# Performance work log

Hardware: AMD Instinct MI355X
Metric: run time of the kernel (lower is better)

Reference implementation:

```python
import jax, jax.numpy as jnp
import numpy as np

N_NODES = 100000
N_EDGES = 1600000
D_IN, D_HID, D_OUT = 256, 512, 48
K_STEPS = 10
ALPHA = 0.1


def setup_inputs() -> dict:
    key = jax.random.key(0)
    k_x, k_e, k_w1, k_w2 = jax.random.split(key, 4)
    x = jax.random.normal(k_x, (N_NODES, D_IN), dtype=jnp.float32)
    edge_index = jax.random.randint(k_e, (2, N_EDGES), 0, N_NODES, dtype=jnp.int64)
    # MLP params (Kaiming-ish scaling)
    W1 = jax.random.normal(k_w1, (D_IN, D_HID), dtype=jnp.float32) * (1.0 / np.sqrt(D_IN))
    b1 = jnp.zeros((D_HID,), dtype=jnp.float32)
    W2 = jax.random.normal(k_w2, (D_HID, D_OUT), dtype=jnp.float32) * (1.0 / np.sqrt(D_HID))
    b2 = jnp.zeros((D_OUT,), dtype=jnp.float32)
    return {"x": x, "edge_index": edge_index, "W1": W1, "b1": b1, "W2": W2, "b2": b2}


def reference(x, edge_index, W1, b1, W2, b2):
    N = x.shape[0]
    # --- MLP encoder ---
    h = jax.nn.relu(x @ W1 + b1) @ W2 + b2  # [N, D_OUT]

    # --- APPNP propagation (PyG defaults: add self-loops, symmetric gcn_norm) ---
    loop = jnp.arange(N, dtype=edge_index.dtype)
    src = jnp.concatenate([edge_index[0], loop])  # [E+N]
    dst = jnp.concatenate([edge_index[1], loop])
    ones = jnp.ones(src.shape[0], dtype=h.dtype)
    deg = jax.ops.segment_sum(ones, dst, num_segments=N)  # in-degree incl. self-loop
    dinv = jnp.where(deg > 0, jax.lax.rsqrt(deg), 0.0)
    norm = dinv[src] * dinv[dst]  # [E+N]

    out = h
    for _ in range(K_STEPS):
        msg = out[src] * norm[:, None]                      # gather + scale
        agg = jax.ops.segment_sum(msg, dst, num_segments=N)  # scatter-add
        out = (1.0 - ALPHA) * agg + ALPHA * h                # teleport mix
    return out
```

## Files before the change

### kernel.cpp

```cpp
#include <hip/hip_runtime.h>
#include <hip/hip_fp16.h>

constexpr int D_IN = 256, D_HID = 512, D_OUT = 48;
constexpr int HPAD = 64;
constexpr int K_STEPS = 10;

typedef __attribute__((ext_vector_type(8))) __bf16 bf16x8;
typedef __attribute__((ext_vector_type(4))) float f32x4;

__device__ __forceinline__ unsigned short f2bf(float f) {
  unsigned u = __builtin_bit_cast(unsigned, f);
  u += 0x7fffu + ((u >> 16) & 1u);
  return (unsigned short)(u >> 16);
}


__global__ void zero2_kernel(int* __restrict__ a, int* __restrict__ b, int N) {
  int i = blockIdx.x * 256 + threadIdx.x;
  if (i < N) { a[i] = 0; b[i] = 0; }
}

__global__ void count_kernel(const int* __restrict__ dst, int* __restrict__ cnt, int E) {
  int e = blockIdx.x * 256 + threadIdx.x;
  if (e < E) atomicAdd(&cnt[dst[e]], 1);
}

__global__ void dinv_kernel(const int* __restrict__ cnt, float* __restrict__ dinv, int N) {
  int n = blockIdx.x * 256 + threadIdx.x;
  if (n < N) dinv[n] = rsqrtf((float)(cnt[n] + 1));
}

__global__ void scan1_kernel(const int* __restrict__ cnt, int* __restrict__ row_ptr,
                             int* __restrict__ bsum, int N) {
  __shared__ int sd[256];
  int tid = threadIdx.x, b = blockIdx.x;
  int i0 = b * 1024 + tid * 4;
  int v[4];
#pragma unroll
  for (int m = 0; m < 4; ++m) v[m] = (i0 + m < N) ? ((cnt[i0 + m] + 3) & ~3) : 0;
  int s = v[0] + v[1] + v[2] + v[3];
  sd[tid] = s;
  __syncthreads();
  for (int off = 1; off < 256; off <<= 1) {
    int t = (tid >= off) ? sd[tid - off] : 0;
    __syncthreads();
    sd[tid] += t;
    __syncthreads();
  }
  int run = sd[tid] - s;
#pragma unroll
  for (int m = 0; m < 4; ++m) {
    if (i0 + m < N) row_ptr[i0 + m] = run;
    run += v[m];
  }
  if (tid == 255) bsum[b] = sd[255];
}

__global__ void scan2_kernel(const int* __restrict__ bsum, int* __restrict__ bofs,
                             int* __restrict__ row_ptr, int NB, int N) {
  __shared__ int sd[128];
  int tid = threadIdx.x;
  int v = (tid < NB) ? bsum[tid] : 0;
  sd[tid] = v;
  __syncthreads();
  for (int off = 1; off < 128; off <<= 1) {
    int t = (tid >= off) ? sd[tid - off] : 0;
    __syncthreads();
    sd[tid] += t;
    __syncthreads();
  }
  if (tid < NB) bofs[tid] = sd[tid] - v;
  if (tid == 127) row_ptr[N] = sd[127];
}

__global__ void scan3_kernel(int* __restrict__ row_ptr, const int* __restrict__ bofs, int N) {
  int b = blockIdx.x;
  if (b == 0) return;
  int add = bofs[b];
  int i0 = b * 1024 + threadIdx.x * 4;
#pragma unroll
  for (int m = 0; m < 4; ++m)
    if (i0 + m < N) row_ptr[i0 + m] += add;
}

__global__ void fill_kernel(const int* __restrict__ src, const int* __restrict__ dst,
                            const int* __restrict__ row_ptr, int* __restrict__ cnt2,
                            const float* __restrict__ dinv,
                            int2* __restrict__ edges, int E) {
  int e = blockIdx.x * 256 + threadIdx.x;
  if (e >= E) return;
  int s = src[e], d = dst[e];
  int p = row_ptr[d] + atomicAdd(&cnt2[d], 1);
  edges[p] = make_int2(s, __float_as_int(dinv[s]));
}

__global__ void pad_kernel(const int* __restrict__ cnt, const int* __restrict__ row_ptr,
                           int2* __restrict__ edges, int N) {
  int n = blockIdx.x * 256 + threadIdx.x;
  if (n >= N) return;
  int a = row_ptr[n] + cnt[n];
  int b = row_ptr[n + 1];
  for (int p = a; p < b; ++p) edges[p] = make_int2(n, 0);
}


__global__ void convert_w1(const float* __restrict__ W1, unsigned short* __restrict__ W1T) {
  int i = blockIdx.x * 256 + threadIdx.x;
  if (i >= D_HID * D_IN) return;
  int c = i >> 8, k = i & 255;
  W1T[i] = f2bf(W1[k * D_HID + c]);
}

__global__ void convert_w2(const float* __restrict__ W2, unsigned short* __restrict__ W2T) {
  int i = blockIdx.x * 256 + threadIdx.x;
  if (i >= D_OUT * D_HID) return;
  int n = i >> 9, k = i & 511;
  W2T[i] = f2bf(W2[k * D_OUT + n]);
}


__global__ __launch_bounds__(256, 3) void encoder_kernel(
    const float* __restrict__ x, const float* __restrict__ b1,
    const float* __restrict__ b2,
    const unsigned short* __restrict__ W1T,
    const unsigned short* __restrict__ W2T,
    __half* __restrict__ h2, int N) {
  __shared__ unsigned short sB[64][136];
  __shared__ unsigned short sHid[128][72];
  __shared__ unsigned short sW2[48][72];

  int tid = threadIdx.x;
  int w = tid >> 6, lane = tid & 63;
  int q = lane >> 4, l15 = lane & 15;
  int row0 = blockIdx.x * 128;
  int m0 = w * 16;

  bf16x8 axf[2][8];
#pragma unroll
  for (int mt = 0; mt < 2; ++mt) {
    int grow = row0 + mt * 64 + m0 + l15;
    bool rok = grow < N;
    const float* xr = x + (size_t)grow * D_IN;
#pragma unroll
    for (int jb = 0; jb < 8; ++jb) {
      float4 v0 = make_float4(0.f, 0.f, 0.f, 0.f), v1 = v0;
      if (rok) {
        v0 = *(const float4*)(xr + jb * 32 + q * 8);
        v1 = *(const float4*)(xr + jb * 32 + q * 8 + 4);
      }
      union { bf16x8 v; unsigned short s[8]; } u;
      u.s[0] = f2bf(v0.x); u.s[1] = f2bf(v0.y); u.s[2] = f2bf(v0.z); u.s[3] = f2bf(v0.w);
      u.s[4] = f2bf(v1.x); u.s[5] = f2bf(v1.y); u.s[6] = f2bf(v1.z); u.s[7] = f2bf(v1.w);
      axf[mt][jb] = u.v;
    }
  }

  f32x4 hacc[2][3];
#pragma unroll
  for (int mt = 0; mt < 2; ++mt)
#pragma unroll
    for (int t = 0; t < 3; ++t)
#pragma unroll
      for (int r = 0; r < 4; ++r) hacc[mt][t][r] = 0.f;

  for (int ct = 0; ct < 8; ++ct) {
    int c0 = ct * 64;
    f32x4 acc[2][4];
#pragma unroll
    for (int mt = 0; mt < 2; ++mt)
#pragma unroll
      for (int t = 0; t < 4; ++t)
#pragma unroll
        for (int r = 0; r < 4; ++r) acc[mt][t][r] = 0.f;

#pragma unroll
    for (int kh = 0; kh < 2; ++kh) {
      __syncthreads();
#pragma unroll
      for (int i = 0; i < 4; ++i) {
        int id = i * 256 + tid;
        int r = id >> 4, c = id & 15;
        *(uint4*)&sB[r][c * 8] =
            *(const uint4*)(W1T + (size_t)(c0 + r) * D_IN + kh * 128 + c * 8);
      }
      if (kh == 0) {
        int r = tid >> 3, c8 = tid & 7;
        *(uint4*)&sW2[r][c8 * 8] = *(const uint4*)(W2T + (size_t)r * D_HID + c0 + c8 * 8);
        int id = 256 + tid;
        if (id < 384) {
          int r2 = id >> 3, c2 = id & 7;
          *(uint4*)&sW2[r2][c2 * 8] = *(const uint4*)(W2T + (size_t)r2 * D_HID + c0 + c2 * 8);
        }
      }
      __syncthreads();
#pragma unroll
      for (int kb = 0; kb < 4; ++kb) {
#pragma unroll
        for (int tn = 0; tn < 4; ++tn) {
          bf16x8 b = *(const bf16x8*)&sB[tn * 16 + l15][kb * 32 + q * 8];
          acc[0][tn] = __builtin_amdgcn_mfma_f32_16x16x32_bf16(axf[0][kh * 4 + kb], b, acc[0][tn], 0, 0, 0);
          acc[1][tn] = __builtin_amdgcn_mfma_f32_16x16x32_bf16(axf[1][kh * 4 + kb], b, acc[1][tn], 0, 0, 0);
        }
      }
    }
#pragma unroll
    for (int mt = 0; mt < 2; ++mt)
#pragma unroll
      for (int tn = 0; tn < 4; ++tn) {
        int c = tn * 16 + l15;
        float bias = b1[c0 + c];
#pragma unroll
        for (int rg = 0; rg < 4; ++rg) {
          float v = acc[mt][tn][rg] + bias;
          v = v > 0.f ? v : 0.f;
          sHid[mt * 64 + m0 + q * 4 + rg][c] = f2bf(v);
        }
      }
#pragma unroll
    for (int kk = 0; kk < 2; ++kk) {
      bf16x8 a0 = *(const bf16x8*)&sHid[m0 + l15][kk * 32 + q * 8];
      bf16x8 a1 = *(const bf16x8*)&sHid[64 + m0 + l15][kk * 32 + q * 8];
#pragma unroll
      for (int tn = 0; tn < 3; ++tn) {
        bf16x8 b = *(const bf16x8*)&sW2[tn * 16 + l15][kk * 32 + q * 8];
        hacc[0][tn] = __builtin_amdgcn_mfma_f32_16x16x32_bf16(a0, b, hacc[0][tn], 0, 0, 0);
        hacc[1][tn] = __builtin_amdgcn_mfma_f32_16x16x32_bf16(a1, b, hacc[1][tn], 0, 0, 0);
      }
    }
  }
#pragma unroll
  for (int mt = 0; mt < 2; ++mt) {
#pragma unroll
    for (int tn = 0; tn < 3; ++tn) {
      int c = tn * 16 + l15;
      float bias = b2[c];
#pragma unroll
      for (int rg = 0; rg < 4; ++rg) {
        int gr = row0 + mt * 64 + m0 + q * 4 + rg;
        if (gr < N) h2[(size_t)gr * HPAD + c] = __float2half(hacc[mt][tn][rg] + bias);
      }
    }
#pragma unroll
    for (int rg = 0; rg < 4; ++rg) {
      int gr = row0 + mt * 64 + m0 + q * 4 + rg;
      if (gr < N) h2[(size_t)gr * HPAD + 48 + l15] = __float2half(0.f);
    }
  }
}


__global__ __launch_bounds__(256) void prop_kernel(
    const __half* __restrict__ cur, const __half* __restrict__ h2,
    const float* __restrict__ dinv, const int* __restrict__ row_ptr,
    const int2* __restrict__ edges, __half* __restrict__ nxt,
    float* __restrict__ outf, int N, int last) {
  int wid = (blockIdx.x * 256 + threadIdx.x) >> 6;
  int lane = threadIdx.x & 63;
  int half = lane >> 5;
  int slot = (lane >> 3) & 3;
  int s = lane & 7;
  int node = wid * 2 + half;
  bool nok = node < N;
  int p0 = 0, p1 = 0;
  if (nok) { int2 pp = *(const int2*)(row_ptr + node); p0 = pp.x; p1 = pp.y; }
  int d = p1 - p0;
  int dmax = max(d, __shfl_xor(d, 32));
  int nb = dmax >> 2;

  float acc[8];
#pragma unroll
  for (int i = 0; i < 8; ++i) acc[i] = 0.f;

  int p = p0 + slot;
  int2 er = make_int2(0, 0);
  if (nb > 0) er = edges[p];
  for (int b = 0; b < nb; ++b) {
    float wgt = (p < p1) ? __int_as_float(er.y) : 0.f;
    int sn = er.x;
    int2 ern = er;
    if (b + 1 < nb) ern = edges[p + 4];
    union { float4 f; __half2 h[4]; } u;
    u.f = *(const float4*)(cur + ((size_t)sn << 6) + s * 8);
#pragma unroll
    for (int i = 0; i < 4; ++i) {
      float2 f = __half22float2(u.h[i]);
      acc[2 * i]     += wgt * f.x;
      acc[2 * i + 1] += wgt * f.y;
    }
    er = ern; p += 4;
  }
#pragma unroll
  for (int i = 0; i < 8; ++i) {
    acc[i] += __int_as_float(__builtin_amdgcn_ds_swizzle(__float_as_int(acc[i]), 0x201F));
    acc[i] += __int_as_float(__builtin_amdgcn_ds_swizzle(__float_as_int(acc[i]), 0x401F));
  }
  if ((lane & 24) != 0 || !nok) return;
  float di = dinv[node];
  size_t base = ((size_t)node << 6) + s * 8;
  union { float4 f; __half2 h[4]; } us, uh;
  us.f = *(const float4*)(cur + base);
  uh.f = *(const float4*)(h2 + base);
  float dii = di * di;
  float outv[8];
#pragma unroll
  for (int i = 0; i < 4; ++i) {
    float2 sf = __half22float2(us.h[i]);
    float2 hf = __half22float2(uh.h[i]);
    outv[2 * i]     = 0.9f * (di * acc[2 * i]     + dii * sf.x) + 0.1f * hf.x;
    outv[2 * i + 1] = 0.9f * (di * acc[2 * i + 1] + dii * sf.y) + 0.1f * hf.y;
  }
  if (last) {
    if (s < 6) {
      float* op = outf + (size_t)node * D_OUT + s * 8;
      *(float4*)op       = make_float4(outv[0], outv[1], outv[2], outv[3]);
      *(float4*)(op + 4) = make_float4(outv[4], outv[5], outv[6], outv[7]);
    }
  } else {
    union { uint4 u4; __half2 h[4]; } o;
#pragma unroll
    for (int i = 0; i < 4; ++i) o.h[i] = __floats2half2_rn(outv[2 * i], outv[2 * i + 1]);
    *(uint4*)(nxt + base) = o.u4;
  }
}


extern "C" void kernel_launch(void* const* d_in, const int* in_sizes, int n_in,
                              void* d_out, int out_size, void* d_ws, size_t ws_size,
                              hipStream_t stream) {
  (void)n_in; (void)out_size; (void)ws_size;
  const float* x  = (const float*)d_in[0];
  const int*   ei = (const int*)d_in[1];
  const float* W1 = (const float*)d_in[2];
  const float* b1 = (const float*)d_in[3];
  const float* W2 = (const float*)d_in[4];
  const float* b2 = (const float*)d_in[5];
  const int N = in_sizes[0] / D_IN;
  const int E = in_sizes[1] / 2;
  const int* e_src = ei;
  const int* e_dst = ei + E;

  char* ws = (char*)d_ws;
  size_t off = 0;
  auto take = [&](size_t bytes) -> char* {
    char* p = ws + off;
    off += (bytes + 511) & ~(size_t)511;
    return p;
  };
  int* cnt      = (int*)take((size_t)N * 4);
  int* cnt2     = (int*)take((size_t)N * 4);
  float* dinv   = (float*)take((size_t)N * 4);
  int* row_ptr  = (int*)take((size_t)(N + 1) * 4);
  int* bsum     = (int*)take(1024);
  int* bofs     = (int*)take(1024);
  int2* edges   = (int2*)take(((size_t)E + 4 * (size_t)N) * 8);
  unsigned short* W1T = (unsigned short*)take((size_t)D_IN * D_HID * 2);
  unsigned short* W2T = (unsigned short*)take((size_t)D_HID * D_OUT * 2);
  __half* h2    = (__half*)take((size_t)N * HPAD * 2);
  __half* bufA  = (__half*)take((size_t)N * HPAD * 2);
  __half* bufB  = (__half*)d_out;
  float* outp   = (float*)d_out;

  int nb256 = (N + 255) / 256;
  int eb256 = (E + 255) / 256;
  int NB    = (N + 1023) / 1024;

  zero2_kernel<<<nb256, 256, 0, stream>>>(cnt, cnt2, N);
  count_kernel<<<eb256, 256, 0, stream>>>(e_dst, cnt, E);
  dinv_kernel<<<nb256, 256, 0, stream>>>(cnt, dinv, N);
  scan1_kernel<<<NB, 256, 0, stream>>>(cnt, row_ptr, bsum, N);
  scan2_kernel<<<1, 128, 0, stream>>>(bsum, bofs, row_ptr, NB, N);
  scan3_kernel<<<NB, 256, 0, stream>>>(row_ptr, bofs, N);
  fill_kernel<<<eb256, 256, 0, stream>>>(e_src, e_dst, row_ptr, cnt2, dinv, edges, E);
  pad_kernel<<<nb256, 256, 0, stream>>>(cnt, row_ptr, edges, N);

  convert_w1<<<(D_IN * D_HID + 255) / 256, 256, 0, stream>>>(W1, W1T);
  convert_w2<<<(D_HID * D_OUT + 255) / 256, 256, 0, stream>>>(W2, W2T);
  encoder_kernel<<<(N + 127) / 128, 256, 0, stream>>>(x, b1, b2, W1T, W2T, h2, N);

  int waves = (N + 1) / 2;
  int pblocks = (waves + 3) / 4;
  const __half* src = h2;
  __half* dst = bufA;
  for (int it = 1; it <= K_STEPS; ++it) {
    int last = (it == K_STEPS);
    prop_kernel<<<pblocks, 256, 0, stream>>>(src, h2, dinv, row_ptr, edges,
                                             dst, outp, N, last);
    src = dst;
    dst = (dst == bufA) ? bufB : bufA;
  }
}
```

Before: 749.0 us.

## Drop feature padding to 48 halves, pre-cast x to bf16, prefetch encoder weights

Node feature buffers shrink from a 64-half padded stride to a dense 48-half stride. Each propagation gather now reads 12 bytes per lane instead of 16, and the gather loop is unrolled by two edges to keep more loads in flight. The input x is converted to bf16 in a separate kernel before the encoder, and the encoder's W1/W2 tile loads are software-prefetched into registers one stage ahead. The pre-cast adds an extra full pass over x (read fp32, write bf16). The uint3 loads are narrower and not 16-byte aligned, which may lower gather efficiency.

```diff
diff --git a/kernel.cpp b/kernel.cpp
--- a/kernel.cpp
+++ b/kernel.cpp
@@ -2,7 +2,6 @@
 #include <hip/hip_fp16.h>
 
 constexpr int D_IN = 256, D_HID = 512, D_OUT = 48;
-constexpr int HPAD = 64;
 constexpr int K_STEPS = 10;
 
 typedef __attribute__((ext_vector_type(8))) __bf16 bf16x8;
@@ -104,6 +103,17 @@
 }
 
 
+__global__ void xcast_kernel(const float* __restrict__ x,
+                             unsigned short* __restrict__ xb, int total8) {
+  int i = blockIdx.x * 256 + threadIdx.x;
+  if (i >= total8) return;
+  const float4* p = (const float4*)(x + (size_t)i * 8);
+  float4 a = p[0], b = p[1];
+  unsigned short o[8] = {f2bf(a.x), f2bf(a.y), f2bf(a.z), f2bf(a.w),
+                         f2bf(b.x), f2bf(b.y), f2bf(b.z), f2bf(b.w)};
+  *(uint4*)(xb + (size_t)i * 8) = *(const uint4*)o;
+}
+
 __global__ void convert_w1(const float* __restrict__ W1, unsigned short* __restrict__ W1T) {
   int i = blockIdx.x * 256 + threadIdx.x;
   if (i >= D_HID * D_IN) return;
@@ -120,8 +130,8 @@
 
 
 __global__ __launch_bounds__(256, 3) void encoder_kernel(
-    const float* __restrict__ x, const float* __restrict__ b1,
-    const float* __restrict__ b2,
+    const unsigned short* __restrict__ xb,
+    const float* __restrict__ b1, const float* __restrict__ b2,
     const unsigned short* __restrict__ W1T,
     const unsigned short* __restrict__ W2T,
     __half* __restrict__ h2, int N) {
@@ -134,102 +144,112 @@
   int q = lane >> 4, l15 = lane & 15;
   int row0 = blockIdx.x * 128;
   int m0 = w * 16;
-
-  bf16x8 axf[2][8];
+  int sr = tid >> 4, sc = tid & 15;
+  int w2r0 = tid >> 3, w2c0 = tid & 7;
+  int w2id1 = 256 + tid;
+
+  uint4 axu[2][8];
 #pragma unroll
   for (int mt = 0; mt < 2; ++mt) {
     int grow = row0 + mt * 64 + m0 + l15;
     bool rok = grow < N;
-    const float* xr = x + (size_t)grow * D_IN;
-#pragma unroll
-    for (int jb = 0; jb < 8; ++jb) {
-      float4 v0 = make_float4(0.f, 0.f, 0.f, 0.f), v1 = v0;
-      if (rok) {
-        v0 = *(const float4*)(xr + jb * 32 + q * 8);
-        v1 = *(const float4*)(xr + jb * 32 + q * 8 + 4);
+    const unsigned short* xr = xb + (size_t)grow * D_IN;
+#pragma unroll
+    for (int jb = 0; jb < 8; ++jb)
+      axu[mt][jb] = rok ? *(const uint4*)(xr + jb * 32 + q * 8)
+                        : make_uint4(0, 0, 0, 0);
+  }
+
+  uint4 pre[4], w2p[2];
+#pragma unroll
+  for (int i = 0; i < 4; ++i)
+    pre[i] = *(const uint4*)(W1T + (size_t)(sr + i * 16) * D_IN + sc * 8);
+  w2p[0] = *(const uint4*)(W2T + (size_t)w2r0 * D_HID + w2c0 * 8);
+  if (w2id1 < 384)
+    w2p[1] = *(const uint4*)(W2T + (size_t)(w2id1 >> 3) * D_HID + (w2id1 & 7) * 8);
+
+  f32x4 hacc[2][3];
+#pragma unroll
+  for (int mt = 0; mt < 2; ++mt)
+#pragma unroll
+    for (int t = 0; t < 3; ++t)
+#pragma unroll
+      for (int r = 0; r < 4; ++r) hacc[mt][t][r] = 0.f;
+
+  f32x4 acc[2][4];
+  for (int st = 0; st < 16; ++st) {
+    int ct = st >> 1, kh = st & 1;
+    int c0 = ct * 64;
+    __syncthreads();
+#pragma unroll
+    for (int i = 0; i < 4; ++i)
+      *(uint4*)&sB[sr + i * 16][sc * 8] = pre[i];
+    if (kh == 0) {
+      *(uint4*)&sW2[w2r0][w2c0 * 8] = w2p[0];
+      if (w2id1 < 384) *(uint4*)&sW2[w2id1 >> 3][(w2id1 & 7) * 8] = w2p[1];
+    }
+    __syncthreads();
+    if (st < 15) {
+      int ct2 = (st + 1) >> 1, kh2 = (st + 1) & 1;
+      const unsigned short* wb = W1T + (size_t)(ct2 * 64) * D_IN + kh2 * 128;
+#pragma unroll
+      for (int i = 0; i < 4; ++i)
+        pre[i] = *(const uint4*)(wb + (size_t)(sr + i * 16) * D_IN + sc * 8);
+      if (kh2 == 0) {
+        int c02 = ct2 * 64;
+        w2p[0] = *(const uint4*)(W2T + (size_t)w2r0 * D_HID + c02 + w2c0 * 8);
+        if (w2id1 < 384)
+          w2p[1] = *(const uint4*)(W2T + (size_t)(w2id1 >> 3) * D_HID + c02 + (w2id1 & 7) * 8);
       }
-      union { bf16x8 v; unsigned short s[8]; } u;
-      u.s[0] = f2bf(v0.x); u.s[1] = f2bf(v0.y); u.s[2] = f2bf(v0.z); u.s[3] = f2bf(v0.w);
-      u.s[4] = f2bf(v1.x); u.s[5] = f2bf(v1.y); u.s[6] = f2bf(v1.z); u.s[7] = f2bf(v1.w);
-      axf[mt][jb] = u.v;
-    }
-  }
-
-  f32x4 hacc[2][3];
-#pragma unroll
-  for (int mt = 0; mt < 2; ++mt)
-#pragma unroll
-    for (int t = 0; t < 3; ++t)
-#pragma unroll
-      for (int r = 0; r < 4; ++r) hacc[mt][t][r] = 0.f;
-
-  for (int ct = 0; ct < 8; ++ct) {
-    int c0 = ct * 64;
-    f32x4 acc[2][4];
-#pragma unroll
-    for (int mt = 0; mt < 2; ++mt)
-#pragma unroll
-      for (int t = 0; t < 4; ++t)
-#pragma unroll
-        for (int r = 0; r < 4; ++r) acc[mt][t][r] = 0.f;
-
-#pragma unroll
-    for (int kh = 0; kh < 2; ++kh) {
-      __syncthreads();
-#pragma unroll
-      for (int i = 0; i < 4; ++i) {
-        int id = i * 256 + tid;
-        int r = id >> 4, c = id & 15;
-        *(uint4*)&sB[r][c * 8] =
-            *(const uint4*)(W1T + (size_t)(c0 + r) * D_IN + kh * 128 + c * 8);
+    }
+    if (kh == 0) {
+#pragma unroll
+      for (int mt = 0; mt < 2; ++mt)
+#pragma unroll
+        for (int t = 0; t < 4; ++t)
+#pragma unroll
+          for (int r = 0; r < 4; ++r) acc[mt][t][r] = 0.f;
+    }
+#pragma unroll
+    for (int kb = 0; kb < 4; ++kb) {
+      bf16x8 a0 = __builtin_bit_cast(bf16x8, axu[0][kh * 4 + kb]);
+      bf16x8 a1 = __builtin_bit_cast(bf16x8, axu[1][kh * 4 + kb]);
+#pragma unroll
+      for (int tn = 0; tn < 4; ++tn) {
+        bf16x8 b = *(const bf16x8*)&sB[tn * 16 + l15][kb * 32 + q * 8];
+        acc[0][tn] = __builtin_amdgcn_mfma_f32_16x16x32_bf16(a0, b, acc[0][tn], 0, 0, 0);
+        acc[1][tn] = __builtin_amdgcn_mfma_f32_16x16x32_bf16(a1, b, acc[1][tn], 0, 0, 0);
       }
-      if (kh == 0) {
-        int r = tid >> 3, c8 = tid & 7;
-        *(uint4*)&sW2[r][c8 * 8] = *(const uint4*)(W2T + (size_t)r * D_HID + c0 + c8 * 8);
-        int id = 256 + tid;
-        if (id < 384) {
-          int r2 = id >> 3, c2 = id & 7;
-          *(uint4*)&sW2[r2][c2 * 8] = *(const uint4*)(W2T + (size_t)r2 * D_HID + c0 + c2 * 8);
+    }
+    if (kh == 1) {
+#pragma unroll
+      for (int mt = 0; mt < 2; ++mt)
+#pragma unroll
+        for (int tn = 0; tn < 4; ++tn) {
+          int c = tn * 16 + l15;
+          float bias = b1[c0 + c];
+#pragma unroll
+          for (int rg = 0; rg < 4; ++rg) {
+            float v = acc[mt][tn][rg] + bias;
+            v = v > 0.f ? v : 0.f;
+            sHid[mt * 64 + m0 + q * 4 + rg][c] = f2bf(v);
+          }
+        }
+#pragma unroll
+      for (int kk = 0; kk < 2; ++kk) {
+        bf16x8 a0 = *(const bf16x8*)&sHid[m0 + l15][kk * 32 + q * 8];
+        bf16x8 a1 = *(const bf16x8*)&sHid[64 + m0 + l15][kk * 32 + q * 8];
+#pragma unroll
+        for (int tn = 0; tn < 3; ++tn) {
+          bf16x8 b = *(const bf16x8*)&sW2[tn * 16 + l15][kk * 32 + q * 8];
+          hacc[0][tn] = __builtin_amdgcn_mfma_f32_16x16x32_bf16(a0, b, hacc[0][tn], 0, 0, 0);
+          hacc[1][tn] = __builtin_amdgcn_mfma_f32_16x16x32_bf16(a1, b, hacc[1][tn], 0, 0, 0);
         }
       }
-      __syncthreads();
-#pragma unroll
-      for (int kb = 0; kb < 4; ++kb) {
-#pragma unroll
-        for (int tn = 0; tn < 4; ++tn) {
-          bf16x8 b = *(const bf16x8*)&sB[tn * 16 + l15][kb * 32 + q * 8];
-          acc[0][tn] = __builtin_amdgcn_mfma_f32_16x16x32_bf16(axf[0][kh * 4 + kb], b, acc[0][tn], 0, 0, 0);
-          acc[1][tn] = __builtin_amdgcn_mfma_f32_16x16x32_bf16(axf[1][kh * 4 + kb], b, acc[1][tn], 0, 0, 0);
-        }
-      }
-    }
-#pragma unroll
-    for (int mt = 0; mt < 2; ++mt)
-#pragma unroll
-      for (int tn = 0; tn < 4; ++tn) {
-        int c = tn * 16 + l15;
-        float bias = b1[c0 + c];
-#pragma unroll
-        for (int rg = 0; rg < 4; ++rg) {
-          float v = acc[mt][tn][rg] + bias;
-          v = v > 0.f ? v : 0.f;
-          sHid[mt * 64 + m0 + q * 4 + rg][c] = f2bf(v);
-        }
-      }
-#pragma unroll
-    for (int kk = 0; kk < 2; ++kk) {
-      bf16x8 a0 = *(const bf16x8*)&sHid[m0 + l15][kk * 32 + q * 8];
-      bf16x8 a1 = *(const bf16x8*)&sHid[64 + m0 + l15][kk * 32 + q * 8];
-#pragma unroll
-      for (int tn = 0; tn < 3; ++tn) {
-        bf16x8 b = *(const bf16x8*)&sW2[tn * 16 + l15][kk * 32 + q * 8];
-        hacc[0][tn] = __builtin_amdgcn_mfma_f32_16x16x32_bf16(a0, b, hacc[0][tn], 0, 0, 0);
-        hacc[1][tn] = __builtin_amdgcn_mfma_f32_16x16x32_bf16(a1, b, hacc[1][tn], 0, 0, 0);
-      }
-    }
-  }
-#pragma unroll
-  for (int mt = 0; mt < 2; ++mt) {
+    }
+  }
+#pragma unroll
+  for (int mt = 0; mt < 2; ++mt)
 #pragma unroll
     for (int tn = 0; tn < 3; ++tn) {
       int c = tn * 16 + l15;
@@ -237,17 +257,20 @@
 #pragma unroll
       for (int rg = 0; rg < 4; ++rg) {
         int gr = row0 + mt * 64 + m0 + q * 4 + rg;
-        if (gr < N) h2[(size_t)gr * HPAD + c] = __float2half(hacc[mt][tn][rg] + bias);
+        if (gr < N) h2[(size_t)gr * D_OUT + c] = __float2half(hacc[mt][tn][rg] + bias);
       }
     }
-#pragma unroll
-    for (int rg = 0; rg < 4; ++rg) {
-      int gr = row0 + mt * 64 + m0 + q * 4 + rg;
-      if (gr < N) h2[(size_t)gr * HPAD + 48 + l15] = __float2half(0.f);
-    }
-  }
-}
-
+}
+
+
+__device__ __forceinline__ void fma6(float* acc, float wgt, uint3 g) {
+  float2 f0 = __half22float2(__builtin_bit_cast(__half2, g.x));
+  float2 f1 = __half22float2(__builtin_bit_cast(__half2, g.y));
+  float2 f2 = __half22float2(__builtin_bit_cast(__half2, g.z));
+  acc[0] += wgt * f0.x; acc[1] += wgt * f0.y;
+  acc[2] += wgt * f1.x; acc[3] += wgt * f1.y;
+  acc[4] += wgt * f2.x; acc[5] += wgt * f2.y;
+}
 
 __global__ __launch_bounds__(256) void prop_kernel(
     const __half* __restrict__ cur, const __half* __restrict__ h2,
@@ -267,59 +290,68 @@
   int dmax = max(d, __shfl_xor(d, 32));
   int nb = dmax >> 2;
 
-  float acc[8];
-#pragma unroll
-  for (int i = 0; i < 8; ++i) acc[i] = 0.f;
+  float acc[6];
+#pragma unroll
+  for (int i = 0; i < 6; ++i) acc[i] = 0.f;
 
   int p = p0 + slot;
-  int2 er = make_int2(0, 0);
-  if (nb > 0) er = edges[p];
-  for (int b = 0; b < nb; ++b) {
-    float wgt = (p < p1) ? __int_as_float(er.y) : 0.f;
-    int sn = er.x;
-    int2 ern = er;
-    if (b + 1 < nb) ern = edges[p + 4];
-    union { float4 f; __half2 h[4]; } u;
-    u.f = *(const float4*)(cur + ((size_t)sn << 6) + s * 8);
-#pragma unroll
-    for (int i = 0; i < 4; ++i) {
-      float2 f = __half22float2(u.h[i]);
-      acc[2 * i]     += wgt * f.x;
-      acc[2 * i + 1] += wgt * f.y;
-    }
-    er = ern; p += 4;
-  }
-#pragma unroll
-  for (int i = 0; i < 8; ++i) {
+  int2 e0 = make_int2(0, 0), e1 = make_int2(0, 0);
+  if (nb > 0) e0 = edges[p];
+  if (nb > 1) e1 = edges[p + 4];
+  int b = 0;
+  for (; b + 2 <= nb; b += 2) {
+    int2 n0 = make_int2(0, 0), n1 = make_int2(0, 0);
+    if (b + 2 < nb) n0 = edges[p + 8];
+    if (b + 3 < nb) n1 = edges[p + 12];
+    float w0 = (p < p1) ? __int_as_float(e0.y) : 0.f;
+    float w1 = (p + 4 < p1) ? __int_as_float(e1.y) : 0.f;
+    uint3 g0 = *(const uint3*)(cur + (size_t)e0.x * 48 + s * 6);
+    uint3 g1 = *(const uint3*)(cur + (size_t)e1.x * 48 + s * 6);
+    fma6(acc, w0, g0);
+    fma6(acc, w1, g1);
+    e0 = n0; e1 = n1; p += 8;
+  }
+  if (b < nb) {
+    float w0 = (p < p1) ? __int_as_float(e0.y) : 0.f;
+    uint3 g0 = *(const uint3*)(cur + (size_t)e0.x * 48 + s * 6);
+    fma6(acc, w0, g0);
+  }
+#pragma unroll
+  for (int i = 0; i < 6; ++i) {
     acc[i] += __int_as_float(__builtin_amdgcn_ds_swizzle(__float_as_int(acc[i]), 0x201F));
     acc[i] += __int_as_float(__builtin_amdgcn_ds_swizzle(__float_as_int(acc[i]), 0x401F));
   }
   if ((lane & 24) != 0 || !nok) return;
   float di = dinv[node];
-  size_t base = ((size_t)node << 6) + s * 8;
-  union { float4 f; __half2 h[4]; } us, uh;
-  us.f = *(const float4*)(cur + base);
-  uh.f = *(const float4*)(h2 + base);
+  size_t base = (size_t)node * 48 + s * 6;
+  uint3 su = *(const uint3*)(cur + base);
+  uint3 hu = *(const uint3*)(h2 + base);
   float dii = di * di;
-  float outv[8];
-#pragma unroll
-  for (int i = 0; i < 4; ++i) {
-    float2 sf = __half22float2(us.h[i]);
-    float2 hf = __half22float2(uh.h[i]);
-    outv[2 * i]     = 0.9f * (di * acc[2 * i]     + dii * sf.x) + 0.1f * hf.x;
-    outv[2 * i + 1] = 0.9f * (di * acc[2 * i + 1] + dii * sf.y) + 0.1f * hf.y;
-  }
+  float sf[6], hf[6];
+  {
+    float2 t;
+    t = __half22float2(__builtin_bit_cast(__half2, su.x)); sf[0] = t.x; sf[1] = t.y;
+    t = __half22float2(__builtin_bit_cast(__half2, su.y)); sf[2] = t.x; sf[3] = t.y;
+    t = __half22float2(__builtin_bit_cast(__half2, su.z)); sf[4] = t.x; sf[5] = t.y;
+    t = __half22float2(__builtin_bit_cast(__half2, hu.x)); hf[0] = t.x; hf[1] = t.y;
+    t = __half22float2(__builtin_bit_cast(__half2, hu.y)); hf[2] = t.x; hf[3] = t.y;
+    t = __half22float2(__builtin_bit_cast(__half2, hu.z)); hf[4] = t.x; hf[5] = t.y;
+  }
+  float outv[6];
+#pragma unroll
+  for (int i = 0; i < 6; ++i)
+    outv[i] = 0.9f * (di * acc[i] + dii * sf[i]) + 0.1f * hf[i];
   if (last) {
-    if (s < 6) {
-      float* op = outf + (size_t)node * D_OUT + s * 8;
-      *(float4*)op       = make_float4(outv[0], outv[1], outv[2], outv[3]);
-      *(float4*)(op + 4) = make_float4(outv[4], outv[5], outv[6], outv[7]);
-    }
+    float* op = outf + base;
+    *(float2*)op       = make_float2(outv[0], outv[1]);
+    *(float2*)(op + 2) = make_float2(outv[2], outv[3]);
+    *(float2*)(op + 4) = make_float2(outv[4], outv[5]);
   } else {
-    union { uint4 u4; __half2 h[4]; } o;
-#pragma unroll
-    for (int i = 0; i < 4; ++i) o.h[i] = __floats2half2_rn(outv[2 * i], outv[2 * i + 1]);
-    *(uint4*)(nxt + base) = o.u4;
+    uint3 o;
+    o.x = __builtin_bit_cast(unsigned, __floats2half2_rn(outv[0], outv[1]));
+    o.y = __builtin_bit_cast(unsigned, __floats2half2_rn(outv[2], outv[3]));
+    o.z = __builtin_bit_cast(unsigned, __floats2half2_rn(outv[4], outv[5]));
+    *(uint3*)(nxt + base) = o;
   }
 }
 
@@ -353,10 +385,11 @@
   int* bsum     = (int*)take(1024);
   int* bofs     = (int*)take(1024);
   int2* edges   = (int2*)take(((size_t)E + 4 * (size_t)N) * 8);
+  unsigned short* xb  = (unsigned short*)take((size_t)N * D_IN * 2);
   unsigned short* W1T = (unsigned short*)take((size_t)D_IN * D_HID * 2);
   unsigned short* W2T = (unsigned short*)take((size_t)D_HID * D_OUT * 2);
-  __half* h2    = (__half*)take((size_t)N * HPAD * 2);
-  __half* bufA  = (__half*)take((size_t)N * HPAD * 2);
+  __half* h2    = (__half*)take((size_t)N * D_OUT * 2);
+  __half* bufA  = (__half*)take((size_t)N * D_OUT * 2);
   __half* bufB  = (__half*)d_out;
   float* outp   = (float*)d_out;
 
@@ -373,9 +406,11 @@
   fill_kernel<<<eb256, 256, 0, stream>>>(e_src, e_dst, row_ptr, cnt2, dinv, edges, E);
   pad_kernel<<<nb256, 256, 0, stream>>>(cnt, row_ptr, edges, N);
 
+  int total8 = N * D_IN / 8;
+  xcast_kernel<<<(total8 + 255) / 256, 256, 0, stream>>>(x, xb, total8);
   convert_w1<<<(D_IN * D_HID + 255) / 256, 256, 0, stream>>>(W1, W1T);
   convert_w2<<<(D_HID * D_OUT + 255) / 256, 256, 0, stream>>>(W2, W2T);
-  encoder_kernel<<<(N + 127) / 128, 256, 0, stream>>>(x, b1, b2, W1T, W2T, h2, N);
+  encoder_kernel<<<(N + 127) / 128, 256, 0, stream>>>(xb, b1, b2, W1T, W2T, h2, N);
 
   int waves = (N + 1) / 2;
   int pblocks = (waves + 3) / 4;
```

Result: slower. 884.8 us (+18.1%).

## Pre-swizzle weights into MFMA fragment order and unroll propagation gather by two

Applied to the files above, without the earlier changes.

Weights are converted into a layout that matches the MFMA B-fragment lane order. Each encoder wave then loads its operands directly from global/L2 memory, with no shared-memory staging or block barriers, and sHid becomes per-wave. The propagation loop now handles two edges per iteration, with two independent row gathers in flight and the edge records prefetched two ahead. The encoder gives up LDS reuse of the weights in exchange for repeated global reads from cache, and the launch bound drops to two blocks per CU.

```diff
diff --git a/kernel.cpp b/kernel.cpp
--- a/kernel.cpp
+++ b/kernel.cpp
@@ -104,41 +104,46 @@
 }
 
 
-__global__ void convert_w1(const float* __restrict__ W1, unsigned short* __restrict__ W1T) {
+__global__ void convert_w1(const float* __restrict__ W1, unsigned short* __restrict__ W1F) {
   int i = blockIdx.x * 256 + threadIdx.x;
   if (i >= D_HID * D_IN) return;
   int c = i >> 8, k = i & 255;
-  W1T[i] = f2bf(W1[k * D_HID + c]);
-}
-
-__global__ void convert_w2(const float* __restrict__ W2, unsigned short* __restrict__ W2T) {
+  int ct = c >> 6, tn = (c >> 4) & 3, l15 = c & 15;
+  int kb = k >> 5, q = (k >> 3) & 3, j = k & 7;
+  int lane = (q << 4) | l15;
+  int dst = (((ct * 4 + tn) * 8 + kb) << 9) + lane * 8 + j;
+  W1F[dst] = f2bf(W1[k * D_HID + c]);
+}
+
+__global__ void convert_w2(const float* __restrict__ W2, unsigned short* __restrict__ W2F) {
   int i = blockIdx.x * 256 + threadIdx.x;
   if (i >= D_OUT * D_HID) return;
   int n = i >> 9, k = i & 511;
-  W2T[i] = f2bf(W2[k * D_OUT + n]);
-}
-
-
-__global__ __launch_bounds__(256, 3) void encoder_kernel(
+  int ct = k >> 6, kk = (k >> 5) & 1, q = (k >> 3) & 3, j = k & 7;
+  int tn = n >> 4, l15 = n & 15;
+  int lane = (q << 4) | l15;
+  int dst = (((ct * 2 + kk) * 3 + tn) << 9) + lane * 8 + j;
+  W2F[dst] = f2bf(W2[k * D_OUT + n]);
+}
+
+
+__global__ __launch_bounds__(256, 2) void encoder_kernel(
     const float* __restrict__ x, const float* __restrict__ b1,
     const float* __restrict__ b2,
-    const unsigned short* __restrict__ W1T,
-    const unsigned short* __restrict__ W2T,
+    const unsigned short* __restrict__ W1F,
+    const unsigned short* __restrict__ W2F,
     __half* __restrict__ h2, int N) {
-  __shared__ unsigned short sB[64][136];
-  __shared__ unsigned short sHid[128][72];
-  __shared__ unsigned short sW2[48][72];
+  __shared__ unsigned short sHid[4][2][16][72];
 
   int tid = threadIdx.x;
   int w = tid >> 6, lane = tid & 63;
   int q = lane >> 4, l15 = lane & 15;
-  int row0 = blockIdx.x * 128;
-  int m0 = w * 16;
-
-  bf16x8 axf[2][8];
+  int row0 = blockIdx.x * 128 + w * 32;
+
+  uint4 axu[2][8];
 #pragma unroll
   for (int mt = 0; mt < 2; ++mt) {
-    int grow = row0 + mt * 64 + m0 + l15;
+    int grow = row0 + mt * 16 + l15;
     bool rok = grow < N;
     const float* xr = x + (size_t)grow * D_IN;
 #pragma unroll
@@ -148,10 +153,10 @@
         v0 = *(const float4*)(xr + jb * 32 + q * 8);
         v1 = *(const float4*)(xr + jb * 32 + q * 8 + 4);
       }
-      union { bf16x8 v; unsigned short s[8]; } u;
-      u.s[0] = f2bf(v0.x); u.s[1] = f2bf(v0.y); u.s[2] = f2bf(v0.z); u.s[3] = f2bf(v0.w);
-      u.s[4] = f2bf(v1.x); u.s[5] = f2bf(v1.y); u.s[6] = f2bf(v1.z); u.s[7] = f2bf(v1.w);
-      axf[mt][jb] = u.v;
+      union { uint4 u; unsigned short s[8]; } uu;
+      uu.s[0] = f2bf(v0.x); uu.s[1] = f2bf(v0.y); uu.s[2] = f2bf(v0.z); uu.s[3] = f2bf(v0.w);
+      uu.s[4] = f2bf(v1.x); uu.s[5] = f2bf(v1.y); uu.s[6] = f2bf(v1.z); uu.s[7] = f2bf(v1.w);
+      axu[mt][jb] = uu.u;
     }
   }
 
@@ -173,35 +178,23 @@
 #pragma unroll
         for (int r = 0; r < 4; ++r) acc[mt][t][r] = 0.f;
 
-#pragma unroll
-    for (int kh = 0; kh < 2; ++kh) {
-      __syncthreads();
-#pragma unroll
-      for (int i = 0; i < 4; ++i) {
-        int id = i * 256 + tid;
-        int r = id >> 4, c = id & 15;
-        *(uint4*)&sB[r][c * 8] =
-            *(const uint4*)(W1T + (size_t)(c0 + r) * D_IN + kh * 128 + c * 8);
-      }
-      if (kh == 0) {
-        int r = tid >> 3, c8 = tid & 7;
-        *(uint4*)&sW2[r][c8 * 8] = *(const uint4*)(W2T + (size_t)r * D_HID + c0 + c8 * 8);
-        int id = 256 + tid;
-        if (id < 384) {
-          int r2 = id >> 3, c2 = id & 7;
-          *(uint4*)&sW2[r2][c2 * 8] = *(const uint4*)(W2T + (size_t)r2 * D_HID + c0 + c2 * 8);
-        }
-      }
-      __syncthreads();
-#pragma unroll
-      for (int kb = 0; kb < 4; ++kb) {
-#pragma unroll
-        for (int tn = 0; tn < 4; ++tn) {
-          bf16x8 b = *(const bf16x8*)&sB[tn * 16 + l15][kb * 32 + q * 8];
-          acc[0][tn] = __builtin_amdgcn_mfma_f32_16x16x32_bf16(axf[0][kh * 4 + kb], b, acc[0][tn], 0, 0, 0);
-          acc[1][tn] = __builtin_amdgcn_mfma_f32_16x16x32_bf16(axf[1][kh * 4 + kb], b, acc[1][tn], 0, 0, 0);
-        }
-      }
+    const unsigned short* wbase = W1F + ((size_t)(ct * 4) << 12) + lane * 8;
+#pragma unroll
+    for (int kb = 0; kb < 8; ++kb) {
+      uint4 bq0 = *(const uint4*)(wbase + (kb << 9));
+      uint4 bq1 = *(const uint4*)(wbase + (kb << 9) + 4096);
+      uint4 bq2 = *(const uint4*)(wbase + (kb << 9) + 8192);
+      uint4 bq3 = *(const uint4*)(wbase + (kb << 9) + 12288);
+      bf16x8 a0 = __builtin_bit_cast(bf16x8, axu[0][kb]);
+      bf16x8 a1 = __builtin_bit_cast(bf16x8, axu[1][kb]);
+      acc[0][0] = __builtin_amdgcn_mfma_f32_16x16x32_bf16(a0, __builtin_bit_cast(bf16x8, bq0), acc[0][0], 0, 0, 0);
+      acc[1][0] = __builtin_amdgcn_mfma_f32_16x16x32_bf16(a1, __builtin_bit_cast(bf16x8, bq0), acc[1][0], 0, 0, 0);
+      acc[0][1] = __builtin_amdgcn_mfma_f32_16x16x32_bf16(a0, __builtin_bit_cast(bf16x8, bq1), acc[0][1], 0, 0, 0);
+      acc[1][1] = __builtin_amdgcn_mfma_f32_16x16x32_bf16(a1, __builtin_bit_cast(bf16x8, bq1), acc[1][1], 0, 0, 0);
+      acc[0][2] = __builtin_amdgcn_mfma_f32_16x16x32_bf16(a0, __builtin_bit_cast(bf16x8, bq2), acc[0][2], 0, 0, 0);
+      acc[1][2] = __builtin_amdgcn_mfma_f32_16x16x32_bf16(a1, __builtin_bit_cast(bf16x8, bq2), acc[1][2], 0, 0, 0);
+      acc[0][3] = __builtin_amdgcn_mfma_f32_16x16x32_bf16(a0, __builtin_bit_cast(bf16x8, bq3), acc[0][3], 0, 0, 0);
+      acc[1][3] = __builtin_amdgcn_mfma_f32_16x16x32_bf16(a1, __builtin_bit_cast(bf16x8, bq3), acc[1][3], 0, 0, 0);
     }
 #pragma unroll
     for (int mt = 0; mt < 2; ++mt)
@@ -213,16 +206,17 @@
         for (int rg = 0; rg < 4; ++rg) {
           float v = acc[mt][tn][rg] + bias;
           v = v > 0.f ? v : 0.f;
-          sHid[mt * 64 + m0 + q * 4 + rg][c] = f2bf(v);
+          sHid[w][mt][q * 4 + rg][c] = f2bf(v);
         }
       }
 #pragma unroll
     for (int kk = 0; kk < 2; ++kk) {
-      bf16x8 a0 = *(const bf16x8*)&sHid[m0 + l15][kk * 32 + q * 8];
-      bf16x8 a1 = *(const bf16x8*)&sHid[64 + m0 + l15][kk * 32 + q * 8];
+      bf16x8 a0 = *(const bf16x8*)&sHid[w][0][l15][kk * 32 + q * 8];
+      bf16x8 a1 = *(const bf16x8*)&sHid[w][1][l15][kk * 32 + q * 8];
+      const unsigned short* w2b = W2F + (((ct * 2 + kk) * 3) << 9) + lane * 8;
 #pragma unroll
       for (int tn = 0; tn < 3; ++tn) {
-        bf16x8 b = *(const bf16x8*)&sW2[tn * 16 + l15][kk * 32 + q * 8];
+        bf16x8 b = *(const bf16x8*)(w2b + (tn << 9));
         hacc[0][tn] = __builtin_amdgcn_mfma_f32_16x16x32_bf16(a0, b, hacc[0][tn], 0, 0, 0);
         hacc[1][tn] = __builtin_amdgcn_mfma_f32_16x16x32_bf16(a1, b, hacc[1][tn], 0, 0, 0);
       }
@@ -236,13 +230,13 @@
       float bias = b2[c];
 #pragma unroll
       for (int rg = 0; rg < 4; ++rg) {
-        int gr = row0 + mt * 64 + m0 + q * 4 + rg;
+        int gr = row0 + mt * 16 + q * 4 + rg;
         if (gr < N) h2[(size_t)gr * HPAD + c] = __float2half(hacc[mt][tn][rg] + bias);
       }
     }
 #pragma unroll
     for (int rg = 0; rg < 4; ++rg) {
-      int gr = row0 + mt * 64 + m0 + q * 4 + rg;
+      int gr = row0 + mt * 16 + q * 4 + rg;
       if (gr < N) h2[(size_t)gr * HPAD + 48 + l15] = __float2half(0.f);
     }
   }
@@ -272,22 +266,38 @@
   for (int i = 0; i < 8; ++i) acc[i] = 0.f;
 
   int p = p0 + slot;
-  int2 er = make_int2(0, 0);
-  if (nb > 0) er = edges[p];
-  for (int b = 0; b < nb; ++b) {
-    float wgt = (p < p1) ? __int_as_float(er.y) : 0.f;
-    int sn = er.x;
-    int2 ern = er;
-    if (b + 1 < nb) ern = edges[p + 4];
-    union { float4 f; __half2 h[4]; } u;
-    u.f = *(const float4*)(cur + ((size_t)sn << 6) + s * 8);
+  int2 e0 = make_int2(0, 0), e1 = make_int2(0, 0);
+  if (nb > 0) e0 = edges[p];
+  if (nb > 1) e1 = edges[p + 4];
+  int b = 0;
+  for (; b + 2 <= nb; b += 2) {
+    int2 n0 = make_int2(0, 0), n1 = make_int2(0, 0);
+    if (b + 2 < nb) n0 = edges[p + 8];
+    if (b + 3 < nb) n1 = edges[p + 12];
+    float w0 = (p < p1) ? __int_as_float(e0.y) : 0.f;
+    float w1 = (p + 4 < p1) ? __int_as_float(e1.y) : 0.f;
+    union { float4 f; __half2 h[4]; } u0, u1;
+    u0.f = *(const float4*)(cur + ((size_t)e0.x << 6) + s * 8);
+    u1.f = *(const float4*)(cur + ((size_t)e1.x << 6) + s * 8);
 #pragma unroll
     for (int i = 0; i < 4; ++i) {
-      float2 f = __half22float2(u.h[i]);
-      acc[2 * i]     += wgt * f.x;
-      acc[2 * i + 1] += wgt * f.y;
-    }
-    er = ern; p += 4;
+      float2 f0 = __half22float2(u0.h[i]);
+      float2 f1 = __half22float2(u1.h[i]);
+      acc[2 * i]     += w0 * f0.x + w1 * f1.x;
+      acc[2 * i + 1] += w0 * f0.y + w1 * f1.y;
+    }
+    e0 = n0; e1 = n1; p += 8;
+  }
+  if (b < nb) {
+    float w0 = (p < p1) ? __int_as_float(e0.y) : 0.f;
+    union { float4 f; __half2 h[4]; } u0;
+    u0.f = *(const float4*)(cur + ((size_t)e0.x << 6) + s * 8);
+#pragma unroll
+    for (int i = 0; i < 4; ++i) {
+      float2 f0 = __half22float2(u0.h[i]);
+      acc[2 * i]     += w0 * f0.x;
+      acc[2 * i + 1] += w0 * f0.y;
+    }
   }
 #pragma unroll
   for (int i = 0; i < 8; ++i) {
@@ -353,8 +363,8 @@
   int* bsum     = (int*)take(1024);
   int* bofs     = (int*)take(1024);
   int2* edges   = (int2*)take(((size_t)E + 4 * (size_t)N) * 8);
-  unsigned short* W1T = (unsigned short*)take((size_t)D_IN * D_HID * 2);
-  unsigned short* W2T = (unsigned short*)take((size_t)D_HID * D_OUT * 2);
+  unsigned short* W1F = (unsigned short*)take((size_t)D_IN * D_HID * 2);
+  unsigned short* W2F = (unsigned short*)take((size_t)D_HID * D_OUT * 2);
   __half* h2    = (__half*)take((size_t)N * HPAD * 2);
   __half* bufA  = (__half*)take((size_t)N * HPAD * 2);
   __half* bufB  = (__half*)d_out;
@@ -373,9 +383,9 @@
   fill_kernel<<<eb256, 256, 0, stream>>>(e_src, e_dst, row_ptr, cnt2, dinv, edges, E);
   pad_kernel<<<nb256, 256, 0, stream>>>(cnt, row_ptr, edges, N);
 
-  convert_w1<<<(D_IN * D_HID + 255) / 256, 256, 0, stream>>>(W1, W1T);
-  convert_w2<<<(D_HID * D_OUT + 255) / 256, 256, 0, stream>>>(W2, W2T);
-  encoder_kernel<<<(N + 127) / 128, 256, 0, stream>>>(x, b1, b2, W1T, W2T, h2, N);
+  convert_w1<<<(D_IN * D_HID + 255) / 256, 256, 0, stream>>>(W1, W1F);
+  convert_w2<<<(D_HID * D_OUT + 255) / 256, 256, 0, stream>>>(W2, W2F);
+  encoder_kernel<<<(N + 127) / 128, 256, 0, stream>>>(x, b1, b2, W1F, W2F, h2, N);
 
   int waves = (N + 1) / 2;
   int pblocks = (waves + 3) / 4;
```

Result: no change. 743.0 us (-0.8%).
